# Performance work log

Measured on AMD Instinct MI355X. Metric: run time of the kernel, lower is better.

## Reference

```python
import jax, jax.numpy as jnp
import numpy as np

B, S, V, D, H, L = 2, 1024, 32000, 1024, 16, 4
DK = D // H
DF = 4 * D
EPS = 1e-5


def setup_inputs() -> dict:
    key = jax.random.key(0)
    ks = jax.random.split(key, 9)
    s = 0.02
    rn = lambda k, shape: jax.random.normal(k, shape, jnp.float32) * s
    return {
        "input_ids": jax.random.randint(ks[0], (B, S), 0, V, dtype=jnp.int32),
        "emb": rn(ks[1], (V, D)),
        "Wq": rn(ks[2], (L, D, D)),
        "Wk": rn(ks[3], (L, D, D)),
        "Wv": rn(ks[4], (L, D, D)),
        "Wo": rn(ks[5], (L, D, D)),
        "W1": rn(ks[6], (L, D, DF)),
        "b1": jnp.zeros((L, DF), jnp.float32),
        "W2": rn(ks[7], (L, DF, D)),
        "b2": jnp.zeros((L, D), jnp.float32),
        "ln1_g": jnp.ones((L, D), jnp.float32),
        "ln1_b": jnp.zeros((L, D), jnp.float32),
        "ln2_g": jnp.ones((L, D), jnp.float32),
        "ln2_b": jnp.zeros((L, D), jnp.float32),
        "lnf_g": jnp.ones((D,), jnp.float32),
        "lnf_b": jnp.zeros((D,), jnp.float32),
        "head_w": rn(ks[8], (D, V)),
    }


def _ln(x, g, b):
    m = jnp.mean(x, -1, keepdims=True)
    v = jnp.mean(jnp.square(x - m), -1, keepdims=True)
    return (x - m) * jax.lax.rsqrt(v + EPS) * g + b


def _heads(x):
    # [B,S,D] -> [B,H,S,DK]
    return x.reshape(B, S, H, DK).transpose(0, 2, 1, 3)


def _forward(input_ids, emb, Wq, Wk, Wv, Wo, W1, b1, W2, b2,
             ln1_g, ln1_b, ln2_g, ln2_b, lnf_g, lnf_b, head_w):
    x = emb[input_ids]  # [B,S,D]
    # causal mask: position q attends to k <= q (prefill, no past)
    mask = jnp.triu(jnp.full((S, S), -jnp.inf, jnp.float32), k=1)
    scale = 1.0 / np.sqrt(DK).astype(np.float32)

    def block(x, p):
        wq, wk, wv, wo, w1, bb1, w2, bb2, g1, be1, g2, be2 = p
        h = _ln(x, g1, be1)
        q = _heads(h @ wq)
        k = _heads(h @ wk)
        v = _heads(h @ wv)
        scores = jnp.einsum('bhqd,bhkd->bhqk', q, k) * scale + mask
        a = jax.nn.softmax(scores, axis=-1)
        o = jnp.einsum('bhqk,bhkd->bhqd', a, v)
        o = o.transpose(0, 2, 1, 3).reshape(B, S, D) @ wo
        x = x + o
        h2 = _ln(x, g2, be2)
        x = x + jax.nn.gelu(h2 @ w1 + bb1, approximate=False) @ w2 + bb2
        return x, None

    x, _ = jax.lax.scan(block, x, (Wq, Wk, Wv, Wo, W1, b1, W2, b2,
                                   ln1_g, ln1_b, ln2_g, ln2_b))
    logits = _ln(x, lnf_g, lnf_b) @ head_w  # [B,S,V]
    return logits


def reference(input_ids, emb, Wq, Wk, Wv, Wo, W1, b1, W2, b2,
              ln1_g, ln1_b, ln2_g, ln2_b, lnf_g, lnf_b, head_w):
    return _forward(input_ids, emb, Wq, Wk, Wv, Wo, W1, b1, W2, b2,
                    ln1_g, ln1_b, ln2_g, ln2_b, lnf_g, lnf_b, head_w)
```

## Files before the change

kernel.cpp:

```cpp
#include <hip/hip_runtime.h>
#include <stdint.h>

#define B_ 2
#define S_ 1024
#define V_ 32000
#define D_ 1024
#define H_ 16
#define L_ 4
#define DF_ 4096
#define M_ (B_*S_)

typedef short short8 __attribute__((ext_vector_type(8)));
typedef float f32x4 __attribute__((ext_vector_type(4)));

__device__ __forceinline__ unsigned short f2bf(float f){
  union { float f; unsigned int u; } v; v.f = f;
  unsigned int u = v.u;
  u = u + 0x7fffu + ((u >> 16) & 1u);
  return (unsigned short)(u >> 16);
}

__device__ __forceinline__ float bf2f(unsigned short u){
  union { unsigned int u; float f; } v; v.u = ((unsigned int)u) << 16;
  return v.f;
}

__device__ __forceinline__ void gload16(const void* g, void* l){
  __builtin_amdgcn_global_load_lds(
      (__attribute__((address_space(1))) void*)(uintptr_t)g,
      (__attribute__((address_space(3))) void*)(uintptr_t)l, 16, 0, 0);
}

__global__ __launch_bounds__(256) void embed_k(const int* __restrict__ ids,
    const float* __restrict__ emb, float* __restrict__ x){
  int row = blockIdx.x;
  int id = ids[row];
  float4 v = reinterpret_cast<const float4*>(emb + (size_t)id*D_)[threadIdx.x];
  reinterpret_cast<float4*>(x + (size_t)row*D_)[threadIdx.x] = v;
}

__global__ __launch_bounds__(256) void ln_k(const float* __restrict__ x,
    const float* __restrict__ g, const float* __restrict__ b,
    unsigned short* __restrict__ out){
  int row = blockIdx.x;
  int tid = threadIdx.x;
  float4 v = reinterpret_cast<const float4*>(x + (size_t)row*D_)[tid];
  float s = v.x+v.y+v.z+v.w;
  float ss = v.x*v.x + v.y*v.y + v.z*v.z + v.w*v.w;
  #pragma unroll
  for (int off=1; off<64; off<<=1){ s += __shfl_xor(s, off); ss += __shfl_xor(ss, off); }
  __shared__ float rs[4], rss[4];
  int wave = tid>>6, lane = tid&63;
  if (lane==0){ rs[wave]=s; rss[wave]=ss; }
  __syncthreads();
  s  = rs[0]+rs[1]+rs[2]+rs[3];
  ss = rss[0]+rss[1]+rss[2]+rss[3];
  float mean = s * (1.0f/(float)D_);
  float var  = ss * (1.0f/(float)D_) - mean*mean;
  float inv = rsqrtf(var + 1e-5f);
  float4 gg = reinterpret_cast<const float4*>(g)[tid];
  float4 bb = reinterpret_cast<const float4*>(b)[tid];
  ushort4 o;
  o.x = f2bf((v.x-mean)*inv*gg.x + bb.x);
  o.y = f2bf((v.y-mean)*inv*gg.y + bb.y);
  o.z = f2bf((v.z-mean)*inv*gg.z + bb.z);
  o.w = f2bf((v.w-mean)*inv*gg.w + bb.w);
  reinterpret_cast<ushort4*>(out + (size_t)row*D_)[tid] = o;
}

__global__ __launch_bounds__(256) void rln_k(float* __restrict__ x,
    const float* __restrict__ part, const float* __restrict__ bias,
    const float* __restrict__ g, const float* __restrict__ b,
    unsigned short* __restrict__ out, int KS){
  int row = blockIdx.x;
  int tid = threadIdx.x;
  float4 v = reinterpret_cast<const float4*>(x + (size_t)row*D_)[tid];
  for (int z=0; z<KS; z++){
    float4 p = reinterpret_cast<const float4*>(part + (size_t)z*M_*D_ + (size_t)row*D_)[tid];
    v.x+=p.x; v.y+=p.y; v.z+=p.z; v.w+=p.w;
  }
  if (bias){
    float4 bb4 = reinterpret_cast<const float4*>(bias)[tid];
    v.x+=bb4.x; v.y+=bb4.y; v.z+=bb4.z; v.w+=bb4.w;
  }
  reinterpret_cast<float4*>(x + (size_t)row*D_)[tid] = v;
  float s = v.x+v.y+v.z+v.w;
  float ss = v.x*v.x + v.y*v.y + v.z*v.z + v.w*v.w;
  #pragma unroll
  for (int off=1; off<64; off<<=1){ s += __shfl_xor(s, off); ss += __shfl_xor(ss, off); }
  __shared__ float rs[4], rss[4];
  int wave = tid>>6, lane = tid&63;
  if (lane==0){ rs[wave]=s; rss[wave]=ss; }
  __syncthreads();
  s  = rs[0]+rs[1]+rs[2]+rs[3];
  ss = rss[0]+rss[1]+rss[2]+rss[3];
  float mean = s * (1.0f/(float)D_);
  float var  = ss * (1.0f/(float)D_) - mean*mean;
  float inv = rsqrtf(var + 1e-5f);
  float4 gg = reinterpret_cast<const float4*>(g)[tid];
  float4 bb = reinterpret_cast<const float4*>(b)[tid];
  ushort4 o;
  o.x = f2bf((v.x-mean)*inv*gg.x + bb.x);
  o.y = f2bf((v.y-mean)*inv*gg.y + bb.y);
  o.z = f2bf((v.z-mean)*inv*gg.z + bb.z);
  o.w = f2bf((v.w-mean)*inv*gg.w + bb.w);
  reinterpret_cast<ushort4*>(out + (size_t)row*D_)[tid] = o;
}

__global__ __launch_bounds__(256) void transpose_k(const float* __restrict__ in,
    unsigned short* __restrict__ out, int K, int N, size_t in_ls, size_t out_ls){
  __shared__ float t[64][65];
  const float* inp = in + (size_t)blockIdx.z*in_ls;
  unsigned short* outp = out + (size_t)blockIdx.z*out_ls;
  int k0 = blockIdx.y*64, n0 = blockIdx.x*64;
  int rr = threadIdx.x >> 4, c4 = (threadIdx.x & 15)*4;
  #pragma unroll
  for (int i=0;i<4;i++){
    float4 v = *reinterpret_cast<const float4*>(inp + (size_t)(k0+rr+i*16)*N + n0 + c4);
    t[rr+i*16][c4+0]=v.x; t[rr+i*16][c4+1]=v.y; t[rr+i*16][c4+2]=v.z; t[rr+i*16][c4+3]=v.w;
  }
  __syncthreads();
  #pragma unroll
  for (int i=0;i<4;i++){
    int n = rr + i*16;
    ushort4 o;
    o.x = f2bf(t[c4+0][n]); o.y = f2bf(t[c4+1][n]);
    o.z = f2bf(t[c4+2][n]); o.w = f2bf(t[c4+3][n]);
    *reinterpret_cast<ushort4*>(outp + (size_t)(n0+n)*K + k0 + c4) = o;
  }
}

#define VMC(n)  asm volatile("s_waitcnt vmcnt(" #n ")" ::: "memory")

template<int EP>
__global__ __launch_bounds__(256)
void gemm_bt(const unsigned short* __restrict__ A, const unsigned short* __restrict__ B,
             void* __restrict__ C, const float* __restrict__ bias,
             const float* __restrict__ resid, int K, int ldc, int MB, int kLen){
  __shared__ unsigned short As[2][128*64];
  __shared__ unsigned short Bs[2][128*64];
  const int tid = threadIdx.x;
  const int wave = tid>>6, lane = tid&63;
  const int wm = wave>>1, wn = wave&1;
  const int nwg = gridDim.x;
  const int p = blockIdx.x;
  const int t = (nwg & 7) ? p : ((p & 7)*(nwg>>3) + (p>>3));
  const int by = t % MB, bx = t / MB;
  const int row0 = by*128, col0 = bx*128;
  const int kz = blockIdx.z;
  const int k0 = kz*kLen;
  f32x4 acc[4][4] = {};
  const int sw8 = ((lane&7) ^ ((lane>>3)&7))*8;
  const unsigned short* Ag = A + (size_t)(row0 + wave*8 + (lane>>3))*K + sw8;
  const unsigned short* Bg = B + (size_t)(col0 + wave*8 + (lane>>3))*K + sw8;
  const int r = lane&15, g16 = lane>>4;
  const int rsw = (r&7)<<4;
#define STAGE_BT(buf, kt) do{ \
    _Pragma("unroll") \
    for (int i=0;i<4;i++){ \
      gload16(Ag + (size_t)i*32*K + (kt), As[buf] + (wave*8 + i*32)*64); \
      gload16(Bg + (size_t)i*32*K + (kt), Bs[buf] + (wave*8 + i*32)*64); \
    } }while(0)
  STAGE_BT(0, k0);
  __syncthreads();
  int cur = 0;
  for (int kt=k0; kt<k0+kLen; kt+=64){
    if (kt + 64 < k0 + kLen) STAGE_BT(cur^1, kt+64);
    #pragma unroll
    for (int ks=0; ks<2; ks++){
      short8 a[4], b[4];
      #pragma unroll
      for (int m=0;m<4;m++)
        a[m] = *reinterpret_cast<const short8*>((const char*)As[cur] + (wm*64+m*16+r)*128 + ((ks*64 + g16*16) ^ rsw));
      #pragma unroll
      for (int n=0;n<4;n++)
        b[n] = *reinterpret_cast<const short8*>((const char*)Bs[cur] + (wn*64+n*16+r)*128 + ((ks*64 + g16*16) ^ rsw));
      #pragma unroll
      for (int m=0;m<4;m++)
        #pragma unroll
        for (int n=0;n<4;n++)
          acc[m][n] = __builtin_amdgcn_mfma_f32_16x16x32_bf16(a[m], b[n], acc[m][n], 0,0,0);
    }
    __syncthreads();
    cur ^= 1;
  }
  #pragma unroll
  for (int m=0;m<4;m++){
    const int row = row0 + wm*64 + m*16 + g16*4;
    #pragma unroll
    for (int n=0;n<4;n++){
      const int col = col0 + wn*64 + n*16 + r;
      #pragma unroll
      for (int j=0;j<4;j++){
        float val = acc[m][n][j];
        size_t idx = (size_t)(row+j)*ldc + col;
        if constexpr (EP==2 || EP==3) val += bias[col];
        if constexpr (EP==2) val = 0.5f*val*(1.0f + erff(val*0.70710678118f));
        if constexpr (EP==1 || EP==3) val += resid[idx];
        if constexpr (EP==0 || EP==2) ((unsigned short*)C)[idx] = f2bf(val);
        else ((float*)C)[idx] = val;
      }
    }
  }
}

#define LDA8(buf,m,ks) (*(const short8*)(lds8 + (buf)*65536 + (wm*128+(m)*16+r)*128 + (((ks)*64+g16*16)^rsw)))
#define LDB8(buf,n,ks) (*(const short8*)(lds8 + (buf)*65536 + 32768 + (wn*64+(n)*16+r)*128 + (((ks)*64+g16*16)^rsw)))
#define STG(buf,isB,h,i,tile) gload16( \
    ((isB) ? Bw + (size_t)(col0 + (h)*128 + (i)*64 + wave*8 + srow)*K + (size_t)(tile)*64 + scsw \
           : A  + (size_t)(row0 + (h)*128 + (i)*64 + wave*8 + srow)*K + (size_t)(tile)*64 + scsw), \
    lds8 + (buf)*65536 + (isB)*32768 + ((h)*128 + (i)*64 + wave*8)*128 )
#define STG_HT(buf,isB,h,tile) do{ STG(buf,isB,h,0,tile); STG(buf,isB,h,1,tile); }while(0)
#define BLOAD8(bT) do{ \
  bfr[0][0]=LDB8(bT,0,0); bfr[0][1]=LDB8(bT,0,1); bfr[1][0]=LDB8(bT,1,0); bfr[1][1]=LDB8(bT,1,1); \
  bfr[2][0]=LDB8(bT,2,0); bfr[2][1]=LDB8(bT,2,1); bfr[3][0]=LDB8(bT,3,0); bfr[3][1]=LDB8(bT,3,1); }while(0)
#define MM8(mb,n) do{ \
  acc[mb][n]    =__builtin_amdgcn_mfma_f32_16x16x32_bf16(a0[0],bfr[n][0],acc[mb][n],0,0,0); \
  acc[mb][n]    =__builtin_amdgcn_mfma_f32_16x16x32_bf16(a0[1],bfr[n][1],acc[mb][n],0,0,0); \
  acc[(mb)+1][n]=__builtin_amdgcn_mfma_f32_16x16x32_bf16(a1[0],bfr[n][0],acc[(mb)+1][n],0,0,0); \
  acc[(mb)+1][n]=__builtin_amdgcn_mfma_f32_16x16x32_bf16(a1[1],bfr[n][1],acc[(mb)+1][n],0,0,0); }while(0)
#define PH8(bT, mb, STAGES, TAIL) do{ \
  short8 a0[2], a1[2]; \
  a0[0]=LDA8(bT,mb,0); a0[1]=LDA8(bT,mb,1); a1[0]=LDA8(bT,(mb)+1,0); a1[1]=LDA8(bT,(mb)+1,1); \
  STAGES; \
  __builtin_amdgcn_s_barrier(); \
  asm volatile("s_waitcnt lgkmcnt(0)" ::: "memory"); \
  __builtin_amdgcn_s_setprio(1); \
  MM8(mb,0); MM8(mb,1); MM8(mb,2); MM8(mb,3); \
  __builtin_amdgcn_s_setprio(0); \
  TAIL; \
  __builtin_amdgcn_s_barrier(); \
}while(0)

__global__ __launch_bounds__(512, 2)
void gemm_8ph(const unsigned short* __restrict__ A, const unsigned short* __restrict__ Bw,
              float* __restrict__ C, int K, int ldc, int MB){
  __shared__ char lds8[131072];
  const int tid = threadIdx.x;
  const int wave = tid>>6, lane = tid&63;
  const int wm = wave>>2, wn = wave&3;
  const int nwg = gridDim.x;
  const int pp = blockIdx.x;
  const int t = (nwg & 7) ? pp : ((pp & 7)*(nwg>>3) + (pp>>3));
  const int by = t % MB, bx = t / MB;
  const int row0 = by*256, col0 = bx*256;
  const int r = lane&15, g16 = lane>>4;
  const int rsw = (r&7)<<4;
  const int srow = lane>>3;
  const int scsw = ((lane&7) ^ srow)*8;

  f32x4 acc[8][4] = {};
  short8 bfr[4][2];
  const int NT = K/64;

  STG_HT(0,1,0,0); STG_HT(0,1,1,0);
  STG_HT(0,0,0,0); STG_HT(0,0,1,0);
  STG_HT(1,1,0,1); STG_HT(1,1,1,1);
  VMC(4);
  __builtin_amdgcn_s_barrier();

  for (int T0 = 0; T0 < NT-2; T0 += 2){
    BLOAD8(0);
    PH8(0, 0, STG_HT(1,0,0,T0+1), ((void)0));
    PH8(0, 2, STG_HT(1,0,1,T0+1), ((void)0));
    PH8(0, 4, STG_HT(0,1,0,T0+2), ((void)0));
    PH8(0, 6, STG_HT(0,1,1,T0+2), VMC(4));
    BLOAD8(1);
    PH8(1, 0, STG_HT(0,0,0,T0+2), ((void)0));
    PH8(1, 2, STG_HT(0,0,1,T0+2), ((void)0));
    PH8(1, 4, STG_HT(1,1,0,T0+3), ((void)0));
    PH8(1, 6, STG_HT(1,1,1,T0+3), VMC(4));
  }
  BLOAD8(0);
  PH8(0, 0, STG_HT(1,0,0,NT-1), ((void)0));
  PH8(0, 2, STG_HT(1,0,1,NT-1), ((void)0));
  PH8(0, 4, ((void)0), ((void)0));
  PH8(0, 6, ((void)0), VMC(0));
  BLOAD8(1);
  PH8(1, 0, ((void)0), ((void)0));
  PH8(1, 2, ((void)0), ((void)0));
  PH8(1, 4, ((void)0), ((void)0));
  PH8(1, 6, ((void)0), ((void)0));

  #pragma unroll
  for (int m=0;m<8;m++){
    const int row = row0 + wm*128 + m*16 + g16*4;
    #pragma unroll
    for (int n=0;n<4;n++){
      const int col = col0 + wn*64 + n*16 + r;
      #pragma unroll
      for (int j=0;j<4;j++)
        C[(size_t)(row+j)*ldc + col] = acc[m][n][j];
    }
  }
}

#define L4A(buf,m,ks) (*(const short8*)(lds4 + (buf)*49152 + (wm*64+(m)*16+r)*128 + (((ks)*64+g16*16)^rsw)))
#define L4B(buf,n,ks) (*(const short8*)(lds4 + (buf)*49152 + 16384 + (wn*64+(n)*16+r)*128 + (((ks)*64+g16*16)^rsw)))
#define STG4A(buf,tile) do{ \
  gload16(A4 + (size_t)(row0 + 0*64 + wave*8 + srow)*K + (size_t)(tile)*64 + scsw, lds4 + (buf)*49152 + (0*64+wave*8)*128); \
  gload16(A4 + (size_t)(row0 + 1*64 + wave*8 + srow)*K + (size_t)(tile)*64 + scsw, lds4 + (buf)*49152 + (1*64+wave*8)*128); }while(0)
#define STG4B(buf,tile) do{ \
  gload16(B4 + (size_t)(col0 + 0*64 + wave*8 + srow)*K + (size_t)(tile)*64 + scsw, lds4 + (buf)*49152 + 16384 + (0*64+wave*8)*128); \
  gload16(B4 + (size_t)(col0 + 1*64 + wave*8 + srow)*K + (size_t)(tile)*64 + scsw, lds4 + (buf)*49152 + 16384 + (1*64+wave*8)*128); \
  gload16(B4 + (size_t)(col0 + 2*64 + wave*8 + srow)*K + (size_t)(tile)*64 + scsw, lds4 + (buf)*49152 + 16384 + (2*64+wave*8)*128); \
  gload16(B4 + (size_t)(col0 + 3*64 + wave*8 + srow)*K + (size_t)(tile)*64 + scsw, lds4 + (buf)*49152 + 16384 + (3*64+wave*8)*128); }while(0)
#define BLOAD4(bT) do{ \
  bfr4[0][0]=L4B(bT,0,0); bfr4[0][1]=L4B(bT,0,1); bfr4[1][0]=L4B(bT,1,0); bfr4[1][1]=L4B(bT,1,1); \
  bfr4[2][0]=L4B(bT,2,0); bfr4[2][1]=L4B(bT,2,1); bfr4[3][0]=L4B(bT,3,0); bfr4[3][1]=L4B(bT,3,1); }while(0)
#define MM44(mb,n) do{ \
  acc[mb][n]    =__builtin_amdgcn_mfma_f32_16x16x32_bf16(a0[0],bfr4[n][0],acc[mb][n],0,0,0); \
  acc[mb][n]    =__builtin_amdgcn_mfma_f32_16x16x32_bf16(a0[1],bfr4[n][1],acc[mb][n],0,0,0); \
  acc[(mb)+1][n]=__builtin_amdgcn_mfma_f32_16x16x32_bf16(a1[0],bfr4[n][0],acc[(mb)+1][n],0,0,0); \
  acc[(mb)+1][n]=__builtin_amdgcn_mfma_f32_16x16x32_bf16(a1[1],bfr4[n][1],acc[(mb)+1][n],0,0,0); }while(0)
#define PH4(bT, mb, STAGES, TAIL) do{ \
  short8 a0[2], a1[2]; \
  a0[0]=L4A(bT,mb,0); a0[1]=L4A(bT,mb,1); a1[0]=L4A(bT,(mb)+1,0); a1[1]=L4A(bT,(mb)+1,1); \
  STAGES; \
  __builtin_amdgcn_s_barrier(); \
  asm volatile("s_waitcnt lgkmcnt(0)" ::: "memory"); \
  __builtin_amdgcn_s_setprio(1); \
  MM44(mb,0); MM44(mb,1); MM44(mb,2); MM44(mb,3); \
  __builtin_amdgcn_s_setprio(0); \
  TAIL; \
  __builtin_amdgcn_s_barrier(); \
}while(0)

template<int EP>
__global__ __launch_bounds__(512, 2)
void gemm_4ph(const unsigned short* __restrict__ A, const unsigned short* __restrict__ Bw,
              void* __restrict__ C, const float* __restrict__ bias,
              int K, int ldc, int MB, int kLen){
  __shared__ char lds4[98304];
  const int tid = threadIdx.x;
  const int wave = tid>>6, lane = tid&63;
  const int wm = wave>>2, wn = wave&3;
  const int nwg = gridDim.x;
  const int pp = blockIdx.x;
  const int t = (nwg & 7) ? pp : ((pp & 7)*(nwg>>3) + (pp>>3));
  const int by = t % MB, bx = t / MB;
  const int row0 = by*128, col0 = bx*256;
  const int r = lane&15, g16 = lane>>4;
  const int rsw = (r&7)<<4;
  const int srow = lane>>3;
  const int scsw = ((lane&7) ^ srow)*8;
  const int kz = blockIdx.z;
  const unsigned short* A4 = A + (size_t)kz*kLen;
  const unsigned short* B4 = Bw + (size_t)kz*kLen;

  f32x4 acc[4][4] = {};
  short8 bfr4[4][2];
  const int NT = kLen/64;

  STG4B(0,0); STG4A(0,0); STG4B(1,1);
  VMC(4);
  __builtin_amdgcn_s_barrier();

  for (int T0 = 0; T0 < NT-2; T0 += 2){
    BLOAD4(0);
    PH4(0, 0, STG4A(1,T0+1), ((void)0));
    PH4(0, 2, STG4B(0,T0+2), VMC(4));
    BLOAD4(1);
    PH4(1, 0, STG4A(0,T0+2), ((void)0));
    PH4(1, 2, STG4B(1,T0+3), VMC(4));
  }
  BLOAD4(0);
  PH4(0, 0, STG4A(1,NT-1), ((void)0));
  PH4(0, 2, ((void)0), VMC(0));
  BLOAD4(1);
  PH4(1, 0, ((void)0), ((void)0));
  PH4(1, 2, ((void)0), ((void)0));

  float* Cp5 = (float*)C + (size_t)kz*M_*ldc;
  #pragma unroll
  for (int m=0;m<4;m++){
    const int row = row0 + wm*64 + m*16 + g16*4;
    #pragma unroll
    for (int n=0;n<4;n++){
      const int col = col0 + wn*64 + n*16 + r;
      #pragma unroll
      for (int j=0;j<4;j++){
        float val = acc[m][n][j];
        size_t idx = (size_t)(row+j)*ldc + col;
        if constexpr (EP==2) { val += bias[col]; val = 0.5f*val*(1.0f + erff(val*0.70710678118f)); }
        if constexpr (EP==0 || EP==2) ((unsigned short*)C)[idx] = f2bf(val);
        else Cp5[idx] = val;
      }
    }
  }
}

__global__ __launch_bounds__(256)
void attn_k(const unsigned short* __restrict__ qkv, unsigned short* __restrict__ o){
  __shared__ unsigned short Ks[2][64*64];
  __shared__ unsigned short Vt[2][64*64];
  __shared__ unsigned short Ps[4*16*64];
  const int tid = threadIdx.x;
  const int wave = tid>>6, lane = tid&63;
  const int qb = blockIdx.x, h = blockIdx.y, b = blockIdx.z;
  const int r = lane&15, g = lane>>4;
  const size_t rowbase = (size_t)b*S_*3*D_;
  const unsigned short* kbase = qkv + rowbase + D_ + h*64;
  const unsigned short* vbase = qkv + rowbase + 2*D_ + h*64;
  short8 qf[2];
  {
    const unsigned short* qp = qkv + rowbase + (size_t)(qb*64 + wave*16 + r)*(3*D_) + h*64 + g*8;
    short8 q0 = *reinterpret_cast<const short8*>(qp);
    short8 q1 = *reinterpret_cast<const short8*>(qp + 32);
    #pragma unroll
    for (int j=0;j<8;j++){
      qf[0][j] = (short)f2bf(bf2f((unsigned short)q0[j])*0.125f);
      qf[1][j] = (short)f2bf(bf2f((unsigned short)q1[j])*0.125f);
    }
  }
  float mrow[4] = {-INFINITY,-INFINITY,-INFINITY,-INFINITY};
  float lrow[4] = {0.f,0.f,0.f,0.f};
  f32x4 oacc[4] = {};
  const int qglob0 = qb*64 + wave*16 + g*4;
  unsigned short* Pw = Ps + wave*16*64;
  uint4 vdr[2];

  const int key8 = tid>>3;
  const int c8   = (tid&7)*8;
  const int kcsw = ((tid&7) ^ (key8&7))*16;

#define KSTG_A(nxt, kt2) do{ \
  gload16((const char*)(kbase + (size_t)((kt2)*64+key8)*(3*D_)) + kcsw, (char*)Ks[nxt] + wave*1024); \
  gload16((const char*)(kbase + (size_t)((kt2)*64+32+key8)*(3*D_)) + kcsw, (char*)Ks[nxt] + 4096 + wave*1024); \
}while(0)
#define VLOAD_A(kt2) do{ \
  vdr[0] = *reinterpret_cast<const uint4*>(vbase + (size_t)((kt2)*64+key8)*(3*D_) + c8); \
  vdr[1] = *reinterpret_cast<const uint4*>(vbase + (size_t)((kt2)*64+32+key8)*(3*D_) + c8); \
}while(0)
#define VSTORE_A(nxt) do{ \
  _Pragma("unroll") \
  for (int i=0;i<2;i++){ \
    int key = i*32 + key8; \
    const unsigned short* ve = reinterpret_cast<const unsigned short*>(&vdr[i]); \
    _Pragma("unroll") \
    for (int j=0;j<8;j++){ \
      int d = c8 + j; \
      int bo2 = (d*128 + key*2) ^ ((d&7)<<4); \
      *reinterpret_cast<unsigned short*>((char*)Vt[nxt] + bo2) = ve[j]; \
    } \
  } }while(0)

  KSTG_A(0, 0);
  VLOAD_A(0);
  VMC(0);
  VSTORE_A(0);
  __syncthreads();

  int cur = 0;
  for (int kt=0; kt<=qb; kt++){
    const bool pf = (kt < qb);
    if (pf){ KSTG_A(cur^1, kt+1); VLOAD_A(kt+1); }
    f32x4 sacc[4] = {};
    #pragma unroll
    for (int ks=0; ks<2; ks++){
      #pragma unroll
      for (int nb=0; nb<4; nb++){
        int key = nb*16 + r;
        int bo = (key*128 + (ks*32+g*8)*2) ^ ((key&7)<<4);
        short8 kf = *reinterpret_cast<const short8*>((char*)Ks[cur] + bo);
        sacc[nb] = __builtin_amdgcn_mfma_f32_16x16x32_bf16(qf[ks], kf, sacc[nb], 0,0,0);
      }
    }
    float sv[4][4];
    float tm[4] = {-INFINITY,-INFINITY,-INFINITY,-INFINITY};
    if (kt == qb){
      #pragma unroll
      for (int nb=0; nb<4; nb++){
        int key = kt*64 + nb*16 + r;
        #pragma unroll
        for (int j=0;j<4;j++){
          float s = (key <= qglob0 + j) ? sacc[nb][j] : -INFINITY;
          sv[nb][j] = s;
          tm[j] = fmaxf(tm[j], s);
        }
      }
    } else {
      #pragma unroll
      for (int nb=0; nb<4; nb++)
        #pragma unroll
        for (int j=0;j<4;j++){
          float s = sacc[nb][j];
          sv[nb][j] = s;
          tm[j] = fmaxf(tm[j], s);
        }
    }
    #pragma unroll
    for (int off=1; off<16; off<<=1){
      #pragma unroll
      for (int j=0;j<4;j++) tm[j] = fmaxf(tm[j], __shfl_xor(tm[j], off));
    }
    int chg = 0;
    float mn[4];
    #pragma unroll
    for (int j=0;j<4;j++){ mn[j] = fmaxf(mrow[j], tm[j]); chg |= (mn[j] > mrow[j]); }
    if (__any(chg)){
      #pragma unroll
      for (int j=0;j<4;j++){
        float sf = __expf(mrow[j]-mn[j]);
        mrow[j] = mn[j];
        lrow[j] *= sf;
        #pragma unroll
        for (int nb=0;nb<4;nb++) oacc[nb][j] *= sf;
      }
    }
    float psum[4] = {0.f,0.f,0.f,0.f};
    #pragma unroll
    for (int nb=0; nb<4; nb++){
      #pragma unroll
      for (int j=0;j<4;j++){
        float p = __expf(sv[nb][j]-mrow[j]);
        psum[j] += p;
        int prow = g*4+j;
        int bo = (prow*128 + (nb*16+r)*2) ^ ((prow&7)<<4);
        *reinterpret_cast<unsigned short*>((char*)Pw + bo) = f2bf(p);
      }
    }
    #pragma unroll
    for (int off=1; off<16; off<<=1){
      #pragma unroll
      for (int j=0;j<4;j++) psum[j] += __shfl_xor(psum[j], off);
    }
    #pragma unroll
    for (int j=0;j<4;j++) lrow[j] += psum[j];
    asm volatile("s_waitcnt lgkmcnt(0)" ::: "memory");
    #pragma unroll
    for (int ks=0; ks<2; ks++){
      int bo = (r*128 + (ks*32+g*8)*2) ^ ((r&7)<<4);
      short8 pf8 = *reinterpret_cast<const short8*>((char*)Pw + bo);
      #pragma unroll
      for (int nb=0; nb<4; nb++){
        int d = nb*16 + r;
        int bo2 = (d*128 + (ks*32+g*8)*2) ^ ((d&7)<<4);
        short8 vf = *reinterpret_cast<const short8*>((char*)Vt[cur] + bo2);
        oacc[nb] = __builtin_amdgcn_mfma_f32_16x16x32_bf16(pf8, vf, oacc[nb], 0,0,0);
      }
    }
    if (pf){ VMC(0); VSTORE_A(cur^1); }
    __syncthreads();
    cur ^= 1;
  }
  #pragma unroll
  for (int nb=0; nb<4; nb++){
    #pragma unroll
    for (int j=0;j<4;j++){
      float ov = oacc[nb][j] / lrow[j];
      size_t row = (size_t)b*S_ + qb*64 + wave*16 + g*4 + j;
      o[row*D_ + h*64 + nb*16 + r] = f2bf(ov);
    }
  }
}

extern "C" void kernel_launch(void* const* d_in, const int* in_sizes, int n_in,
                              void* d_out, int out_size, void* d_ws, size_t ws_size,
                              hipStream_t stream) {
  const int*   ids   = (const int*)  d_in[0];
  const float* emb   = (const float*)d_in[1];
  const float* Wq    = (const float*)d_in[2];
  const float* Wk    = (const float*)d_in[3];
  const float* Wv    = (const float*)d_in[4];
  const float* Wo    = (const float*)d_in[5];
  const float* W1    = (const float*)d_in[6];
  const float* b1    = (const float*)d_in[7];
  const float* W2    = (const float*)d_in[8];
  const float* b2    = (const float*)d_in[9];
  const float* ln1_g = (const float*)d_in[10];
  const float* ln1_b = (const float*)d_in[11];
  const float* ln2_g = (const float*)d_in[12];
  const float* ln2_b = (const float*)d_in[13];
  const float* lnf_g = (const float*)d_in[14];
  const float* lnf_b = (const float*)d_in[15];
  const float* headw = (const float*)d_in[16];

  unsigned short* ws = (unsigned short*)d_ws;
  unsigned short* wqkvT = ws;
  unsigned short* woT   = wqkvT + (size_t)L_*3*D_*D_;
  unsigned short* w1T   = woT   + (size_t)L_*D_*D_;
  unsigned short* w2T   = w1T   + (size_t)L_*D_*DF_;
  unsigned short* headT = w2T   + (size_t)L_*D_*DF_;
  unsigned short* h     = headT + (size_t)V_*D_;
  unsigned short* qkv   = h     + (size_t)M_*D_;
  unsigned short* attno = qkv   + (size_t)M_*3*D_;
  unsigned short* h2    = attno + (size_t)M_*D_;
  float*          x     = (float*)(h2 + (size_t)M_*DF_);
  float*          part  = x + (size_t)M_*D_;
  size_t needed = ((char*)(part + (size_t)4*M_*D_)) - (char*)d_ws;
  const bool splitk = (ws_size >= needed);

  transpose_k<<<dim3(D_/64, D_/64, L_), 256, 0, stream>>>(Wq, wqkvT,            D_, D_, (size_t)D_*D_, (size_t)3*D_*D_);
  transpose_k<<<dim3(D_/64, D_/64, L_), 256, 0, stream>>>(Wk, wqkvT + D_*D_,    D_, D_, (size_t)D_*D_, (size_t)3*D_*D_);
  transpose_k<<<dim3(D_/64, D_/64, L_), 256, 0, stream>>>(Wv, wqkvT + 2*D_*D_,  D_, D_, (size_t)D_*D_, (size_t)3*D_*D_);
  transpose_k<<<dim3(D_/64, D_/64, L_), 256, 0, stream>>>(Wo, woT,              D_, D_, (size_t)D_*D_, (size_t)D_*D_);
  transpose_k<<<dim3(DF_/64, D_/64, L_), 256, 0, stream>>>(W1, w1T,             D_, DF_, (size_t)D_*DF_, (size_t)D_*DF_);
  transpose_k<<<dim3(D_/64, DF_/64, L_), 256, 0, stream>>>(W2, w2T,             DF_, D_, (size_t)D_*DF_, (size_t)D_*DF_);
  transpose_k<<<dim3(V_/64, D_/64, 1), 256, 0, stream>>>(headw, headT,          D_, V_, 0, 0);

  embed_k<<<M_, 256, 0, stream>>>(ids, emb, x);
  ln_k<<<M_, 256, 0, stream>>>(x, ln1_g, ln1_b, h);

  for (int l = 0; l < L_; l++){
    gemm_4ph<0><<<dim3((3*D_/256)*(M_/128), 1, 1), 512, 0, stream>>>(h, wqkvT + (size_t)l*3*D_*D_, qkv, nullptr, D_, 3*D_, M_/128, D_);
    attn_k<<<dim3(S_/64, H_, B_), 256, 0, stream>>>(qkv, attno);
    if (splitk){
      gemm_4ph<5><<<dim3((D_/256)*(M_/128), 1, 4), 512, 0, stream>>>(attno, woT + (size_t)l*D_*D_, part, nullptr, D_, D_, M_/128, D_/4);
      rln_k<<<M_, 256, 0, stream>>>(x, part, nullptr, ln2_g + l*D_, ln2_b + l*D_, h, 4);
    } else {
      gemm_bt<1><<<dim3((D_/128)*(M_/128), 1, 1), 256, 0, stream>>>(attno, woT + (size_t)l*D_*D_, x, nullptr, x, D_, D_, M_/128, D_);
      ln_k<<<M_, 256, 0, stream>>>(x, ln2_g + l*D_, ln2_b + l*D_, h);
    }
    gemm_4ph<2><<<dim3((DF_/256)*(M_/128), 1, 1), 512, 0, stream>>>(h, w1T + (size_t)l*D_*DF_, h2, b1 + l*DF_, D_, DF_, M_/128, D_);
    const float* ng = (l+1 < L_) ? (ln1_g + (l+1)*D_) : lnf_g;
    const float* nb = (l+1 < L_) ? (ln1_b + (l+1)*D_) : lnf_b;
    if (splitk){
      gemm_4ph<5><<<dim3((D_/256)*(M_/128), 1, 4), 512, 0, stream>>>(h2, w2T + (size_t)l*D_*DF_, part, nullptr, DF_, D_, M_/128, DF_/4);
      rln_k<<<M_, 256, 0, stream>>>(x, part, b2 + l*D_, ng, nb, h, 4);
    } else {
      gemm_bt<3><<<dim3((D_/128)*(M_/128), 1, 1), 256, 0, stream>>>(h2, w2T + (size_t)l*D_*DF_, x, b2 + l*D_, x, DF_, D_, M_/128, DF_);
      ln_k<<<M_, 256, 0, stream>>>(x, ng, nb, h);
    }
  }

  gemm_8ph<<<dim3((V_/256)*(M_/256), 1, 1), 512, 0, stream>>>(h, headT, (float*)d_out, D_, V_, M_/256);
}
```

Baseline: 893.9 us.

## Double-buffer A fragments across phases and add 64-row GEMM with 2-way split-K

```diff
diff --git a/kernel.cpp b/kernel.cpp
--- a/kernel.cpp
+++ b/kernel.cpp
@@ -131,6 +131,9 @@
 }
 
 #define VMC(n)  asm volatile("s_waitcnt vmcnt(" #n ")" ::: "memory")
+#define BARW(n) do{ __builtin_amdgcn_s_barrier(); \
+  asm volatile("s_waitcnt lgkmcnt(" #n ")" ::: "memory"); }while(0)
+#define ENDP(TAIL) do{ TAIL; __builtin_amdgcn_s_barrier(); }while(0)
 
 template<int EP>
 __global__ __launch_bounds__(256)
@@ -214,25 +217,18 @@
 #define BLOAD8(bT) do{ \
   bfr[0][0]=LDB8(bT,0,0); bfr[0][1]=LDB8(bT,0,1); bfr[1][0]=LDB8(bT,1,0); bfr[1][1]=LDB8(bT,1,1); \
   bfr[2][0]=LDB8(bT,2,0); bfr[2][1]=LDB8(bT,2,1); bfr[3][0]=LDB8(bT,3,0); bfr[3][1]=LDB8(bT,3,1); }while(0)
-#define MM8(mb,n) do{ \
-  acc[mb][n]    =__builtin_amdgcn_mfma_f32_16x16x32_bf16(a0[0],bfr[n][0],acc[mb][n],0,0,0); \
-  acc[mb][n]    =__builtin_amdgcn_mfma_f32_16x16x32_bf16(a0[1],bfr[n][1],acc[mb][n],0,0,0); \
-  acc[(mb)+1][n]=__builtin_amdgcn_mfma_f32_16x16x32_bf16(a1[0],bfr[n][0],acc[(mb)+1][n],0,0,0); \
-  acc[(mb)+1][n]=__builtin_amdgcn_mfma_f32_16x16x32_bf16(a1[1],bfr[n][1],acc[(mb)+1][n],0,0,0); }while(0)
-#define PH8(bT, mb, STAGES, TAIL) do{ \
-  short8 a0[2], a1[2]; \
-  a0[0]=LDA8(bT,mb,0); a0[1]=LDA8(bT,mb,1); a1[0]=LDA8(bT,(mb)+1,0); a1[1]=LDA8(bT,(mb)+1,1); \
-  STAGES; \
-  __builtin_amdgcn_s_barrier(); \
-  asm volatile("s_waitcnt lgkmcnt(0)" ::: "memory"); \
-  __builtin_amdgcn_s_setprio(1); \
-  MM8(mb,0); MM8(mb,1); MM8(mb,2); MM8(mb,3); \
-  __builtin_amdgcn_s_setprio(0); \
-  TAIL; \
-  __builtin_amdgcn_s_barrier(); \
-}while(0)
-
-__global__ __launch_bounds__(512, 2)
+#define RD_A8(AR,buf,mb) do{ AR[0]=LDA8(buf,mb,0); AR[1]=LDA8(buf,mb,1); \
+                             AR[2]=LDA8(buf,(mb)+1,0); AR[3]=LDA8(buf,(mb)+1,1); }while(0)
+#define MM8A(mb,AR,n) do{ \
+  acc[mb][n]    =__builtin_amdgcn_mfma_f32_16x16x32_bf16(AR[0],bfr[n][0],acc[mb][n],0,0,0); \
+  acc[mb][n]    =__builtin_amdgcn_mfma_f32_16x16x32_bf16(AR[1],bfr[n][1],acc[mb][n],0,0,0); \
+  acc[(mb)+1][n]=__builtin_amdgcn_mfma_f32_16x16x32_bf16(AR[2],bfr[n][0],acc[(mb)+1][n],0,0,0); \
+  acc[(mb)+1][n]=__builtin_amdgcn_mfma_f32_16x16x32_bf16(AR[3],bfr[n][1],acc[(mb)+1][n],0,0,0); }while(0)
+#define MFMA16A(mb,AR) do{ __builtin_amdgcn_s_setprio(1); \
+  MM8A(mb,AR,0); MM8A(mb,AR,1); MM8A(mb,AR,2); MM8A(mb,AR,3); \
+  __builtin_amdgcn_s_setprio(0); }while(0)
+
+__global__ __launch_bounds__(512, 1)
 void gemm_8ph(const unsigned short* __restrict__ A, const unsigned short* __restrict__ Bw,
               float* __restrict__ C, int K, int ldc, int MB){
   __shared__ char lds8[131072];
@@ -251,6 +247,7 @@
 
   f32x4 acc[8][4] = {};
   short8 bfr[4][2];
+  short8 aA[4], aB[4];
   const int NT = K/64;
 
   STG_HT(0,1,0,0); STG_HT(0,1,1,0);
@@ -260,27 +257,27 @@
   __builtin_amdgcn_s_barrier();
 
   for (int T0 = 0; T0 < NT-2; T0 += 2){
-    BLOAD8(0);
-    PH8(0, 0, STG_HT(1,0,0,T0+1), ((void)0));
-    PH8(0, 2, STG_HT(1,0,1,T0+1), ((void)0));
-    PH8(0, 4, STG_HT(0,1,0,T0+2), ((void)0));
-    PH8(0, 6, STG_HT(0,1,1,T0+2), VMC(4));
-    BLOAD8(1);
-    PH8(1, 0, STG_HT(0,0,0,T0+2), ((void)0));
-    PH8(1, 2, STG_HT(0,0,1,T0+2), ((void)0));
-    PH8(1, 4, STG_HT(1,1,0,T0+3), ((void)0));
-    PH8(1, 6, STG_HT(1,1,1,T0+3), VMC(4));
-  }
-  BLOAD8(0);
-  PH8(0, 0, STG_HT(1,0,0,NT-1), ((void)0));
-  PH8(0, 2, STG_HT(1,0,1,NT-1), ((void)0));
-  PH8(0, 4, ((void)0), ((void)0));
-  PH8(0, 6, ((void)0), VMC(0));
-  BLOAD8(1);
-  PH8(1, 0, ((void)0), ((void)0));
-  PH8(1, 2, ((void)0), ((void)0));
-  PH8(1, 4, ((void)0), ((void)0));
-  PH8(1, 6, ((void)0), ((void)0));
+    BLOAD8(0); RD_A8(aA,0,0);
+    RD_A8(aB,0,2); STG_HT(1,0,0,T0+1); BARW(4); MFMA16A(0,aA); ENDP(((void)0));
+    RD_A8(aA,0,4); STG_HT(1,0,1,T0+1); BARW(4); MFMA16A(2,aB); ENDP(((void)0));
+    RD_A8(aB,0,6); STG_HT(0,1,0,T0+2); BARW(4); MFMA16A(4,aA); ENDP(((void)0));
+    STG_HT(0,1,1,T0+2);                BARW(0); MFMA16A(6,aB); ENDP(VMC(4));
+    BLOAD8(1); RD_A8(aA,1,0);
+    RD_A8(aB,1,2); STG_HT(0,0,0,T0+2); BARW(4); MFMA16A(0,aA); ENDP(((void)0));
+    RD_A8(aA,1,4); STG_HT(0,0,1,T0+2); BARW(4); MFMA16A(2,aB); ENDP(((void)0));
+    RD_A8(aB,1,6); STG_HT(1,1,0,T0+3); BARW(4); MFMA16A(4,aA); ENDP(((void)0));
+    STG_HT(1,1,1,T0+3);                BARW(0); MFMA16A(6,aB); ENDP(VMC(4));
+  }
+  BLOAD8(0); RD_A8(aA,0,0);
+  RD_A8(aB,0,2); STG_HT(1,0,0,NT-1); BARW(4); MFMA16A(0,aA); ENDP(((void)0));
+  RD_A8(aA,0,4); STG_HT(1,0,1,NT-1); BARW(4); MFMA16A(2,aB); ENDP(((void)0));
+  RD_A8(aB,0,6);                     BARW(4); MFMA16A(4,aA); ENDP(VMC(0));
+                                     BARW(0); MFMA16A(6,aB); ENDP(((void)0));
+  BLOAD8(1); RD_A8(aA,1,0);
+  RD_A8(aB,1,2);                     BARW(4); MFMA16A(0,aA); ENDP(((void)0));
+  RD_A8(aA,1,4);                     BARW(4); MFMA16A(2,aB); ENDP(((void)0));
+  RD_A8(aB,1,6);                     BARW(4); MFMA16A(4,aA); ENDP(((void)0));
+                                     BARW(0); MFMA16A(6,aB);
 
   #pragma unroll
   for (int m=0;m<8;m++){
@@ -308,26 +305,19 @@
 #define BLOAD4(bT) do{ \
   bfr4[0][0]=L4B(bT,0,0); bfr4[0][1]=L4B(bT,0,1); bfr4[1][0]=L4B(bT,1,0); bfr4[1][1]=L4B(bT,1,1); \
   bfr4[2][0]=L4B(bT,2,0); bfr4[2][1]=L4B(bT,2,1); bfr4[3][0]=L4B(bT,3,0); bfr4[3][1]=L4B(bT,3,1); }while(0)
-#define MM44(mb,n) do{ \
-  acc[mb][n]    =__builtin_amdgcn_mfma_f32_16x16x32_bf16(a0[0],bfr4[n][0],acc[mb][n],0,0,0); \
-  acc[mb][n]    =__builtin_amdgcn_mfma_f32_16x16x32_bf16(a0[1],bfr4[n][1],acc[mb][n],0,0,0); \
-  acc[(mb)+1][n]=__builtin_amdgcn_mfma_f32_16x16x32_bf16(a1[0],bfr4[n][0],acc[(mb)+1][n],0,0,0); \
-  acc[(mb)+1][n]=__builtin_amdgcn_mfma_f32_16x16x32_bf16(a1[1],bfr4[n][1],acc[(mb)+1][n],0,0,0); }while(0)
-#define PH4(bT, mb, STAGES, TAIL) do{ \
-  short8 a0[2], a1[2]; \
-  a0[0]=L4A(bT,mb,0); a0[1]=L4A(bT,mb,1); a1[0]=L4A(bT,(mb)+1,0); a1[1]=L4A(bT,(mb)+1,1); \
-  STAGES; \
-  __builtin_amdgcn_s_barrier(); \
-  asm volatile("s_waitcnt lgkmcnt(0)" ::: "memory"); \
-  __builtin_amdgcn_s_setprio(1); \
-  MM44(mb,0); MM44(mb,1); MM44(mb,2); MM44(mb,3); \
-  __builtin_amdgcn_s_setprio(0); \
-  TAIL; \
-  __builtin_amdgcn_s_barrier(); \
-}while(0)
+#define RD_A4(AR,buf,mb) do{ AR[0]=L4A(buf,mb,0); AR[1]=L4A(buf,mb,1); \
+                             AR[2]=L4A(buf,(mb)+1,0); AR[3]=L4A(buf,(mb)+1,1); }while(0)
+#define MM44A(mb,AR,n) do{ \
+  acc[mb][n]    =__builtin_amdgcn_mfma_f32_16x16x32_bf16(AR[0],bfr4[n][0],acc[mb][n],0,0,0); \
+  acc[mb][n]    =__builtin_amdgcn_mfma_f32_16x16x32_bf16(AR[1],bfr4[n][1],acc[mb][n],0,0,0); \
+  acc[(mb)+1][n]=__builtin_amdgcn_mfma_f32_16x16x32_bf16(AR[2],bfr4[n][0],acc[(mb)+1][n],0,0,0); \
+  acc[(mb)+1][n]=__builtin_amdgcn_mfma_f32_16x16x32_bf16(AR[3],bfr4[n][1],acc[(mb)+1][n],0,0,0); }while(0)
+#define MFMA16A4(mb,AR) do{ __builtin_amdgcn_s_setprio(1); \
+  MM44A(mb,AR,0); MM44A(mb,AR,1); MM44A(mb,AR,2); MM44A(mb,AR,3); \
+  __builtin_amdgcn_s_setprio(0); }while(0)
 
 template<int EP>
-__global__ __launch_bounds__(512, 2)
+__global__ __launch_bounds__(512, 1)
 void gemm_4ph(const unsigned short* __restrict__ A, const unsigned short* __restrict__ Bw,
               void* __restrict__ C, const float* __restrict__ bias,
               int K, int ldc, int MB, int kLen){
@@ -350,6 +340,7 @@
 
   f32x4 acc[4][4] = {};
   short8 bfr4[4][2];
+  short8 aA[4], aB[4];
   const int NT = kLen/64;
 
   STG4B(0,0); STG4A(0,0); STG4B(1,1);
@@ -357,24 +348,110 @@
   __builtin_amdgcn_s_barrier();
 
   for (int T0 = 0; T0 < NT-2; T0 += 2){
-    BLOAD4(0);
-    PH4(0, 0, STG4A(1,T0+1), ((void)0));
-    PH4(0, 2, STG4B(0,T0+2), VMC(4));
-    BLOAD4(1);
-    PH4(1, 0, STG4A(0,T0+2), ((void)0));
-    PH4(1, 2, STG4B(1,T0+3), VMC(4));
-  }
-  BLOAD4(0);
-  PH4(0, 0, STG4A(1,NT-1), ((void)0));
-  PH4(0, 2, ((void)0), VMC(0));
-  BLOAD4(1);
-  PH4(1, 0, ((void)0), ((void)0));
-  PH4(1, 2, ((void)0), ((void)0));
+    BLOAD4(0); RD_A4(aA,0,0);
+    RD_A4(aB,0,2); STG4A(1,T0+1); BARW(4); MFMA16A4(0,aA); ENDP(((void)0));
+    STG4B(0,T0+2);                BARW(0); MFMA16A4(2,aB); ENDP(VMC(4));
+    BLOAD4(1); RD_A4(aA,1,0);
+    RD_A4(aB,1,2); STG4A(0,T0+2); BARW(4); MFMA16A4(0,aA); ENDP(((void)0));
+    STG4B(1,T0+3);                BARW(0); MFMA16A4(2,aB); ENDP(VMC(4));
+  }
+  BLOAD4(0); RD_A4(aA,0,0);
+  RD_A4(aB,0,2); STG4A(1,NT-1);   BARW(4); MFMA16A4(0,aA); ENDP(((void)0));
+                                  BARW(0); MFMA16A4(2,aB); ENDP(VMC(0));
+  BLOAD4(1); RD_A4(aA,1,0);
+  RD_A4(aB,1,2);                  BARW(4); MFMA16A4(0,aA); ENDP(((void)0));
+                                  BARW(0); MFMA16A4(2,aB);
 
   float* Cp5 = (float*)C + (size_t)kz*M_*ldc;
   #pragma unroll
   for (int m=0;m<4;m++){
     const int row = row0 + wm*64 + m*16 + g16*4;
+    #pragma unroll
+    for (int n=0;n<4;n++){
+      const int col = col0 + wn*64 + n*16 + r;
+      #pragma unroll
+      for (int j=0;j<4;j++){
+        float val = acc[m][n][j];
+        size_t idx = (size_t)(row+j)*ldc + col;
+        if constexpr (EP==2) { val += bias[col]; val = 0.5f*val*(1.0f + erff(val*0.70710678118f)); }
+        if constexpr (EP==0 || EP==2) ((unsigned short*)C)[idx] = f2bf(val);
+        else Cp5[idx] = val;
+      }
+    }
+  }
+}
+
+#define L6A(buf,m,ks) (*(const short8*)(lds6 + (buf)*40960 + (wm*32+(m)*16+r)*128 + (((ks)*64+g16*16)^rsw)))
+#define L6B(buf,n,ks) (*(const short8*)(lds6 + (buf)*40960 + 8192 + (wn*64+(n)*16+r)*128 + (((ks)*64+g16*16)^rsw)))
+#define STG6A(buf,tile) \
+  gload16(A6 + (size_t)(row0 + wave*8 + srow)*K + (size_t)(tile)*64 + scsw, lds6 + (buf)*40960 + (wave*8)*128)
+#define STG6B(buf,tile) do{ \
+  gload16(B6 + (size_t)(col0 + 0*64 + wave*8 + srow)*K + (size_t)(tile)*64 + scsw, lds6 + (buf)*40960 + 8192 + (0*64+wave*8)*128); \
+  gload16(B6 + (size_t)(col0 + 1*64 + wave*8 + srow)*K + (size_t)(tile)*64 + scsw, lds6 + (buf)*40960 + 8192 + (1*64+wave*8)*128); \
+  gload16(B6 + (size_t)(col0 + 2*64 + wave*8 + srow)*K + (size_t)(tile)*64 + scsw, lds6 + (buf)*40960 + 8192 + (2*64+wave*8)*128); \
+  gload16(B6 + (size_t)(col0 + 3*64 + wave*8 + srow)*K + (size_t)(tile)*64 + scsw, lds6 + (buf)*40960 + 8192 + (3*64+wave*8)*128); }while(0)
+#define BLOAD6(bT) do{ \
+  bfr6[0][0]=L6B(bT,0,0); bfr6[0][1]=L6B(bT,0,1); bfr6[1][0]=L6B(bT,1,0); bfr6[1][1]=L6B(bT,1,1); \
+  bfr6[2][0]=L6B(bT,2,0); bfr6[2][1]=L6B(bT,2,1); bfr6[3][0]=L6B(bT,3,0); bfr6[3][1]=L6B(bT,3,1); }while(0)
+#define RD_A6(AR,buf,mb) do{ AR[0]=L6A(buf,mb,0); AR[1]=L6A(buf,mb,1); }while(0)
+#define MFMA8A6(mb,AR) do{ __builtin_amdgcn_s_setprio(1); \
+  _Pragma("unroll") \
+  for (int n=0;n<4;n++){ \
+    acc[mb][n]=__builtin_amdgcn_mfma_f32_16x16x32_bf16(AR[0],bfr6[n][0],acc[mb][n],0,0,0); \
+    acc[mb][n]=__builtin_amdgcn_mfma_f32_16x16x32_bf16(AR[1],bfr6[n][1],acc[mb][n],0,0,0); \
+  } \
+  __builtin_amdgcn_s_setprio(0); }while(0)
+
+template<int EP>
+__global__ __launch_bounds__(512, 2)
+void gemm_4ph64(const unsigned short* __restrict__ A, const unsigned short* __restrict__ Bw,
+                void* __restrict__ C, const float* __restrict__ bias,
+                int K, int ldc, int MB, int kLen){
+  __shared__ char lds6[81920];
+  const int tid = threadIdx.x;
+  const int wave = tid>>6, lane = tid&63;
+  const int wm = wave>>2, wn = wave&3;
+  const int nwg = gridDim.x;
+  const int pp = blockIdx.x;
+  const int t = (nwg & 7) ? pp : ((pp & 7)*(nwg>>3) + (pp>>3));
+  const int by = t % MB, bx = t / MB;
+  const int row0 = by*64, col0 = bx*256;
+  const int r = lane&15, g16 = lane>>4;
+  const int rsw = (r&7)<<4;
+  const int srow = lane>>3;
+  const int scsw = ((lane&7) ^ srow)*8;
+  const int kz = blockIdx.z;
+  const unsigned short* A6 = A + (size_t)kz*kLen;
+  const unsigned short* B6 = Bw + (size_t)kz*kLen;
+
+  f32x4 acc[2][4] = {};
+  short8 bfr6[4][2];
+  short8 aA[2], aB[2];
+  const int NT = kLen/64;
+
+  STG6B(0,0); STG6A(0,0); STG6B(1,1);
+  VMC(4);
+  __builtin_amdgcn_s_barrier();
+
+  for (int T0 = 0; T0 < NT-2; T0 += 2){
+    BLOAD6(0); RD_A6(aA,0,0);
+    RD_A6(aB,0,1); STG6A(1,T0+1); BARW(2); MFMA8A6(0,aA); ENDP(((void)0));
+    STG6B(0,T0+2);                BARW(0); MFMA8A6(1,aB); ENDP(VMC(4));
+    BLOAD6(1); RD_A6(aA,1,0);
+    RD_A6(aB,1,1); STG6A(0,T0+2); BARW(2); MFMA8A6(0,aA); ENDP(((void)0));
+    STG6B(1,T0+3);                BARW(0); MFMA8A6(1,aB); ENDP(VMC(4));
+  }
+  BLOAD6(0); RD_A6(aA,0,0);
+  RD_A6(aB,0,1); STG6A(1,NT-1);   BARW(2); MFMA8A6(0,aA); ENDP(((void)0));
+                                  BARW(0); MFMA8A6(1,aB); ENDP(VMC(0));
+  BLOAD6(1); RD_A6(aA,1,0);
+  RD_A6(aB,1,1);                  BARW(2); MFMA8A6(0,aA); ENDP(((void)0));
+                                  BARW(0); MFMA8A6(1,aB);
+
+  float* Cp5 = (float*)C + (size_t)kz*M_*ldc;
+  #pragma unroll
+  for (int m=0;m<2;m++){
+    const int row = row0 + wm*32 + m*16 + g16*4;
     #pragma unroll
     for (int n=0;n<4;n++){
       const int col = col0 + wn*64 + n*16 + r;
@@ -588,7 +665,7 @@
   unsigned short* h2    = attno + (size_t)M_*D_;
   float*          x     = (float*)(h2 + (size_t)M_*DF_);
   float*          part  = x + (size_t)M_*D_;
-  size_t needed = ((char*)(part + (size_t)4*M_*D_)) - (char*)d_ws;
+  size_t needed = ((char*)(part + (size_t)2*M_*D_)) - (char*)d_ws;
   const bool splitk = (ws_size >= needed);
 
   transpose_k<<<dim3(D_/64, D_/64, L_), 256, 0, stream>>>(Wq, wqkvT,            D_, D_, (size_t)D_*D_, (size_t)3*D_*D_);
@@ -603,11 +680,11 @@
   ln_k<<<M_, 256, 0, stream>>>(x, ln1_g, ln1_b, h);
 
   for (int l = 0; l < L_; l++){
-    gemm_4ph<0><<<dim3((3*D_/256)*(M_/128), 1, 1), 512, 0, stream>>>(h, wqkvT + (size_t)l*3*D_*D_, qkv, nullptr, D_, 3*D_, M_/128, D_);
+    gemm_4ph64<0><<<dim3((3*D_/256)*(M_/64), 1, 1), 512, 0, stream>>>(h, wqkvT + (size_t)l*3*D_*D_, qkv, nullptr, D_, 3*D_, M_/64, D_);
     attn_k<<<dim3(S_/64, H_, B_), 256, 0, stream>>>(qkv, attno);
     if (splitk){
-      gemm_4ph<5><<<dim3((D_/256)*(M_/128), 1, 4), 512, 0, stream>>>(attno, woT + (size_t)l*D_*D_, part, nullptr, D_, D_, M_/128, D_/4);
-      rln_k<<<M_, 256, 0, stream>>>(x, part, nullptr, ln2_g + l*D_, ln2_b + l*D_, h, 4);
+      gemm_4ph64<5><<<dim3((D_/256)*(M_/64), 1, 2), 512, 0, stream>>>(attno, woT + (size_t)l*D_*D_, part, nullptr, D_, D_, M_/64, D_/2);
+      rln_k<<<M_, 256, 0, stream>>>(x, part, nullptr, ln2_g + l*D_, ln2_b + l*D_, h, 2);
     } else {
       gemm_bt<1><<<dim3((D_/128)*(M_/128), 1, 1), 256, 0, stream>>>(attno, woT + (size_t)l*D_*D_, x, nullptr, x, D_, D_, M_/128, D_);
       ln_k<<<M_, 256, 0, stream>>>(x, ln2_g + l*D_, ln2_b + l*D_, h);
@@ -616,8 +693,8 @@
     const float* ng = (l+1 < L_) ? (ln1_g + (l+1)*D_) : lnf_g;
     const float* nb = (l+1 < L_) ? (ln1_b + (l+1)*D_) : lnf_b;
     if (splitk){
-      gemm_4ph<5><<<dim3((D_/256)*(M_/128), 1, 4), 512, 0, stream>>>(h2, w2T + (size_t)l*D_*DF_, part, nullptr, DF_, D_, M_/128, DF_/4);
-      rln_k<<<M_, 256, 0, stream>>>(x, part, b2 + l*D_, ng, nb, h, 4);
+      gemm_4ph64<5><<<dim3((D_/256)*(M_/64), 1, 2), 512, 0, stream>>>(h2, w2T + (size_t)l*D_*DF_, part, nullptr, DF_, D_, M_/64, DF_/2);
+      rln_k<<<M_, 256, 0, stream>>>(x, part, b2 + l*D_, ng, nb, h, 2);
     } else {
       gemm_bt<3><<<dim3((D_/128)*(M_/128), 1, 1), 256, 0, stream>>>(h2, w2T + (size_t)l*D_*DF_, x, b2 + l*D_, x, DF_, D_, M_/128, DF_);
       ln_k<<<M_, 256, 0, stream>>>(x, ng, nb, h);
```

Measured after the change: 920.3 us. 1.03x slower.
